# Kernel tuning notes

Hardware: AMD Instinct MI355X
Metric: run time of the kernel (lower is better)

The kernel has to match this reference:

```python
import jax, jax.numpy as jnp
import numpy as np

N_NODES = 100000


def _spmm(edge_src, edge_dst, edge_vals, support):
    # out[i] = sum_{e: dst(e)=i} w_e * support[src(e)]  (sparse adj @ support)
    msgs = support[edge_src] * edge_vals[:, None]  # [E, F]
    return jax.ops.segment_sum(msgs, edge_dst, num_segments=N_NODES)


def setup_inputs() -> dict:
    key = jax.random.key(0)
    ks = jax.random.split(key, 8)
    E = 1600000
    feat_dim, nhid, num_class = 256, 64, 16
    x = jax.random.normal(ks[0], (N_NODES, feat_dim), dtype=jnp.float32)
    edge_src = jax.random.randint(ks[1], (E,), 0, N_NODES, dtype=jnp.int32)
    edge_dst = jax.random.randint(ks[2], (E,), 0, N_NODES, dtype=jnp.int32)
    edge_vals = jax.random.uniform(ks[3], (E,), dtype=jnp.float32)
    # Glorot-style init as in the original GraphConvolution.reset_parameters
    W1 = jax.random.normal(ks[4], (feat_dim, nhid), dtype=jnp.float32) / np.sqrt(feat_dim)
    b1 = jnp.zeros((nhid,), dtype=jnp.float32)
    W2 = jax.random.normal(ks[5], (nhid, num_class), dtype=jnp.float32) / np.sqrt(nhid)
    b2 = jnp.zeros((num_class,), dtype=jnp.float32)
    return {"x": x, "edge_src": edge_src, "edge_dst": edge_dst,
            "edge_vals": edge_vals, "W1": W1, "b1": b1, "W2": W2, "b2": b2}


def reference(x, edge_src, edge_dst, edge_vals, W1, b1, W2, b2):
    # gc1: support = x @ W1 ; out = adj @ support + b1 ; relu
    h = jax.nn.relu(_spmm(edge_src, edge_dst, edge_vals, x @ W1) + b1)
    # dropout is identity in eval mode (training=False)
    # gc2
    logits = _spmm(edge_src, edge_dst, edge_vals, h @ W2) + b2
    return jax.nn.log_softmax(logits, axis=1)
```

## Files before the change

### kernel.cpp

```cpp
#include <hip/hip_runtime.h>
#include <hip/hip_fp16.h>

#define N_NODES 100000
#define E_EDGES 1600000
#define F_IN    256
#define F_HID   64
#define F_OUT   16
#define NBKT    391
#define CAP     4608
#define PA_BLOCKS    391
#define GEMM1_BLOCKS 782

typedef _Float16 half8   __attribute__((ext_vector_type(8)));
typedef float    floatx4 __attribute__((ext_vector_type(4)));

__global__ __launch_bounds__(256) void gemm1_passA_kernel(const float* __restrict__ x,
                                                          const float* __restrict__ W1,
                                                          _Float16* __restrict__ support1,
                                                          const int* __restrict__ esrc,
                                                          const int* __restrict__ edst,
                                                          const float* __restrict__ evals,
                                                          int* __restrict__ bucketCursor,
                                                          int2* __restrict__ tmp) {
    __shared__ __align__(16) char ldsbuf[32768];
    const int t = threadIdx.x;

    if (blockIdx.x >= GEMM1_BLOCKS) {
        int* hist = (int*)ldsbuf;
        int* base = hist + NBKT;
        const int blk = blockIdx.x - GEMM1_BLOCKS;
        for (int i = t; i < NBKT; i += 256) hist[i] = 0;
        __syncthreads();
        const int base_e = blk * 4096;
        int rks[4][4];
#pragma unroll
        for (int ch = 0; ch < 4; ++ch) {
            const int e0 = base_e + ch * 1024 + t * 4;
            if (e0 < E_EDGES) {
                int4 d4 = *(const int4*)&edst[e0];
                rks[ch][0] = atomicAdd(&hist[d4.x >> 8], 1);
                rks[ch][1] = atomicAdd(&hist[d4.y >> 8], 1);
                rks[ch][2] = atomicAdd(&hist[d4.z >> 8], 1);
                rks[ch][3] = atomicAdd(&hist[d4.w >> 8], 1);
            }
        }
        __syncthreads();
        for (int i = t; i < NBKT; i += 256)
            base[i] = atomicAdd(&bucketCursor[i], hist[i]);
        __syncthreads();
#pragma unroll
        for (int ch = 0; ch < 4; ++ch) {
            const int e0 = base_e + ch * 1024 + t * 4;
            if (e0 < E_EDGES) {
                int4 d4 = *(const int4*)&edst[e0];
                int4 s4 = *(const int4*)&esrc[e0];
                float4 v4 = *(const float4*)&evals[e0];
                const int dd[4] = {d4.x, d4.y, d4.z, d4.w};
                const int ss[4] = {s4.x, s4.y, s4.z, s4.w};
                const float vv[4] = {v4.x, v4.y, v4.z, v4.w};
#pragma unroll
                for (int u = 0; u < 4; ++u) {
                    const int bu = dd[u] >> 8;
                    const int bpos = base[bu] + rks[ch][u];
                    if (bpos < CAP)
                        tmp[bu * CAP + bpos] =
                            make_int2(((dd[u] & 255) << 17) | ss[u],
                                      __float_as_int(vv[u]));
                }
            }
        }
        return;
    }

    _Float16* Bs = (_Float16*)ldsbuf;
    for (int i = t; i < 16384; i += 256) {
        const int k = i >> 6, n = i & 63;
        const int kb = k >> 5, quad = (k >> 3) & 3, j = k & 7;
        const int nt = n >> 4, ln = n & 15;
        Bs[((kb * 4 + nt) * 64 + quad * 16 + ln) * 8 + j] = (_Float16)W1[i];
    }
    __syncthreads();

    const int wave = t >> 6;
    const int lane = t & 63;
    const int ln   = lane & 15;
    const int quad = lane >> 4;
    const int row0 = blockIdx.x * 128 + wave * 32;

    const float* xp[2];
#pragma unroll
    for (int mt = 0; mt < 2; ++mt) {
        int r = row0 + mt * 16 + ln;
        if (r > N_NODES - 1) r = N_NODES - 1;
        xp[mt] = x + (size_t)r * F_IN + quad * 8;
    }

    floatx4 acc[2][4] = {};

#pragma unroll 4
    for (int kb = 0; kb < 8; ++kb) {
        half8 a[2];
#pragma unroll
        for (int mt = 0; mt < 2; ++mt) {
            float4 v0 = *(const float4*)(xp[mt] + kb * 32);
            float4 v1 = *(const float4*)(xp[mt] + kb * 32 + 4);
            half8 h;
            h[0] = (_Float16)v0.x; h[1] = (_Float16)v0.y;
            h[2] = (_Float16)v0.z; h[3] = (_Float16)v0.w;
            h[4] = (_Float16)v1.x; h[5] = (_Float16)v1.y;
            h[6] = (_Float16)v1.z; h[7] = (_Float16)v1.w;
            a[mt] = h;
        }
#pragma unroll
        for (int nt = 0; nt < 4; ++nt) {
            half8 b = *(const half8*)&Bs[((size_t)((kb * 4 + nt) * 64 + lane)) * 8];
            acc[0][nt] = __builtin_amdgcn_mfma_f32_16x16x32_f16(a[0], b, acc[0][nt], 0, 0, 0);
            acc[1][nt] = __builtin_amdgcn_mfma_f32_16x16x32_f16(a[1], b, acc[1][nt], 0, 0, 0);
        }
    }

#pragma unroll
    for (int mt = 0; mt < 2; ++mt) {
        const int rbase = row0 + mt * 16 + quad * 4;
#pragma unroll
        for (int r = 0; r < 4; ++r) {
            const int row = rbase + r;
            if (row < N_NODES) {
#pragma unroll
                for (int nt = 0; nt < 4; ++nt)
                    support1[(size_t)row * F_HID + nt * 16 + ln] = (_Float16)acc[mt][nt][r];
            }
        }
    }
}

__global__ __launch_bounds__(256) void passB_kernel(const int2* __restrict__ tmp,
                                                    const int* __restrict__ bucketCursor,
                                                    int2* __restrict__ sorted_edges,
                                                    int* __restrict__ rowstart,
                                                    int* __restrict__ deg) {
    __shared__ int ldeg[256];
    __shared__ int lcur[256];
    __shared__ int s[256];
    const int t = threadIdx.x;
    const int b = blockIdx.x;
    const int beg = b * CAP;
    int cnt = bucketCursor[b];
    if (cnt > CAP) cnt = CAP;

    ldeg[t] = 0;
    __syncthreads();

    for (int p = t; p < cnt; p += 256) {
        int2 r = tmp[beg + p];
        atomicAdd(&ldeg[r.x >> 17], 1);
    }
    __syncthreads();

    const int v = ldeg[t];
    s[t] = v;
    __syncthreads();
#pragma unroll
    for (int off = 1; off < 256; off <<= 1) {
        const int y = (t >= off) ? s[t - off] : 0;
        __syncthreads();
        s[t] += y;
        __syncthreads();
    }
    const int run = s[t] - v;
    lcur[t] = run;
    const int node = b * 256 + t;
    if (node < N_NODES) { rowstart[node] = beg + run; deg[node] = v; }
    __syncthreads();

    for (int p = t; p < cnt; p += 256) {
        int2 r = tmp[beg + p];
        const int pos = beg + atomicAdd(&lcur[r.x >> 17], 1);
        sorted_edges[pos] = make_int2(r.x & 0x1FFFF, r.y);
    }
}

__global__ __launch_bounds__(256) void spmm1_fused_kernel(const int* __restrict__ rowstart,
                                                          const int* __restrict__ deg,
                                                          const int2* __restrict__ sorted_edges,
                                                          const _Float16* __restrict__ support1,
                                                          const float* __restrict__ b1,
                                                          const float* __restrict__ W2,
                                                          _Float16* __restrict__ support2) {
    __shared__ float W2s[64 * 17];
    __shared__ float b1s[64];
    __shared__ __align__(16) float hs[4][64];
    const int t = threadIdx.x;
    for (int i = t; i < 1024; i += 256)
        W2s[(i >> 4) * 17 + (i & 15)] = W2[i];
    if (t < 64) b1s[t] = b1[t];
    __syncthreads();

    const int wave = t >> 6;
    const int lane = t & 63;
    const int node = blockIdx.x * 4 + wave;
    const int c4 = lane & 15;
    const int q  = lane >> 4;

    const int beg = rowstart[node];
    const int cnt = deg[node];

    int   src_l = 0;
    float val_l = 0.f;
    if (lane < cnt) {
        int2 ev = sorted_edges[beg + lane];
        src_l = ev.x;
        val_l = __int_as_float(ev.y);
    }

    float acc0 = 0.f, acc1 = 0.f, acc2 = 0.f, acc3 = 0.f;
    const int kmax  = cnt < 64 ? cnt : 64;
    const int quads = (kmax + 3) >> 2;
    const int qp    = (quads + 3) & ~3;
    for (int k = 0; k < qp; k += 4) {
        float w[4]; uint2 d[4];
#pragma unroll
        for (int u = 0; u < 4; ++u) {
            const int idx = 4 * (k + u) + q;
            const int s2  = __shfl(src_l, idx);
            w[u] = __shfl(val_l, idx);
            d[u] = *(const uint2*)&support1[(size_t)s2 * F_HID + 4 * c4];
        }
#pragma unroll
        for (int u = 0; u < 4; ++u) {
            const _Float16* hp = (const _Float16*)&d[u];
            acc0 = fmaf(w[u], (float)hp[0], acc0);
            acc1 = fmaf(w[u], (float)hp[1], acc1);
            acc2 = fmaf(w[u], (float)hp[2], acc2);
            acc3 = fmaf(w[u], (float)hp[3], acc3);
        }
    }
    for (int k = 64 + q; k < cnt; k += 4) {
        int2 ev = sorted_edges[beg + k];
        const float w = __int_as_float(ev.y);
        const uint2 d = *(const uint2*)&support1[(size_t)ev.x * F_HID + 4 * c4];
        const _Float16* hp = (const _Float16*)&d;
        acc0 = fmaf(w, (float)hp[0], acc0);
        acc1 = fmaf(w, (float)hp[1], acc1);
        acc2 = fmaf(w, (float)hp[2], acc2);
        acc3 = fmaf(w, (float)hp[3], acc3);
    }

    acc0 += __shfl_xor(acc0, 16); acc0 += __shfl_xor(acc0, 32);
    acc1 += __shfl_xor(acc1, 16); acc1 += __shfl_xor(acc1, 32);
    acc2 += __shfl_xor(acc2, 16); acc2 += __shfl_xor(acc2, 32);
    acc3 += __shfl_xor(acc3, 16); acc3 += __shfl_xor(acc3, 32);
    if (q == 0) {
        float4 hv;
        hv.x = fmaxf(acc0 + b1s[4 * c4],     0.f);
        hv.y = fmaxf(acc1 + b1s[4 * c4 + 1], 0.f);
        hv.z = fmaxf(acc2 + b1s[4 * c4 + 2], 0.f);
        hv.w = fmaxf(acc3 + b1s[4 * c4 + 3], 0.f);
        *(float4*)&hs[wave][4 * c4] = hv;
    }
    __syncthreads();

    const int ln   = lane & 15;
    const int quad = lane >> 4;
    float o = 0.f;
#pragma unroll
    for (int kk = 0; kk < 16; ++kk) {
        const int k2 = quad * 16 + kk;
        o = fmaf(hs[wave][k2], W2s[k2 * 17 + ln], o);
    }
    o += __shfl_xor(o, 16);
    o += __shfl_xor(o, 32);
    if (quad == 0)
        support2[(size_t)node * F_OUT + ln] = (_Float16)o;
}

__global__ __launch_bounds__(256) void spmm2_fused_kernel(const int* __restrict__ rowstart,
                                                          const int* __restrict__ deg,
                                                          const int2* __restrict__ sorted_edges,
                                                          const _Float16* __restrict__ support2,
                                                          const float* __restrict__ b2,
                                                          float* __restrict__ out) {
    __shared__ float b2s[16];
    const int t = threadIdx.x;
    if (t < 16) b2s[t] = b2[t];
    __syncthreads();

    const int j    = t & 15;
    const int node = blockIdx.x * 16 + (t >> 4);
    const int c = j & 3;
    const int p = j >> 2;

    const int beg = rowstart[node];
    const int cnt = deg[node];

    int   src_a = 0, src_b = 0;
    float val_a = 0.f, val_b = 0.f;
    if (j < cnt)      { int2 ev = sorted_edges[beg + j];      src_a = ev.x; val_a = __int_as_float(ev.y); }
    if (j + 16 < cnt) { int2 ev = sorted_edges[beg + 16 + j]; src_b = ev.x; val_b = __int_as_float(ev.y); }

    float acc0 = 0.f, acc1 = 0.f, acc2 = 0.f, acc3 = 0.f;
    {
        float w[4]; uint2 d[4];
#pragma unroll
        for (int u = 0; u < 4; ++u) {
            const int idx = 4 * u + p;
            const int s2  = __shfl(src_a, idx, 16);
            w[u] = __shfl(val_a, idx, 16);
            d[u] = *(const uint2*)&support2[(size_t)s2 * F_OUT + 4 * c];
        }
#pragma unroll
        for (int u = 0; u < 4; ++u) {
            const _Float16* hp = (const _Float16*)&d[u];
            acc0 = fmaf(w[u], (float)hp[0], acc0);
            acc1 = fmaf(w[u], (float)hp[1], acc1);
            acc2 = fmaf(w[u], (float)hp[2], acc2);
            acc3 = fmaf(w[u], (float)hp[3], acc3);
        }
    }
    if (cnt > 16) {
        float w[4]; uint2 d[4];
#pragma unroll
        for (int u = 0; u < 4; ++u) {
            const int idx = 4 * u + p;
            const int s2  = __shfl(src_b, idx, 16);
            w[u] = __shfl(val_b, idx, 16);
            d[u] = *(const uint2*)&support2[(size_t)s2 * F_OUT + 4 * c];
        }
#pragma unroll
        for (int u = 0; u < 4; ++u) {
            const _Float16* hp = (const _Float16*)&d[u];
            acc0 = fmaf(w[u], (float)hp[0], acc0);
            acc1 = fmaf(w[u], (float)hp[1], acc1);
            acc2 = fmaf(w[u], (float)hp[2], acc2);
            acc3 = fmaf(w[u], (float)hp[3], acc3);
        }
    }
    for (int k = 32 + p; k < cnt; k += 4) {
        int2 ev = sorted_edges[beg + k];
        const float w = __int_as_float(ev.y);
        const uint2 d = *(const uint2*)&support2[(size_t)ev.x * F_OUT + 4 * c];
        const _Float16* hp = (const _Float16*)&d;
        acc0 = fmaf(w, (float)hp[0], acc0);
        acc1 = fmaf(w, (float)hp[1], acc1);
        acc2 = fmaf(w, (float)hp[2], acc2);
        acc3 = fmaf(w, (float)hp[3], acc3);
    }

    acc0 += __shfl_xor(acc0, 4, 16); acc0 += __shfl_xor(acc0, 8, 16);
    acc1 += __shfl_xor(acc1, 4, 16); acc1 += __shfl_xor(acc1, 8, 16);
    acc2 += __shfl_xor(acc2, 4, 16); acc2 += __shfl_xor(acc2, 8, 16);
    acc3 += __shfl_xor(acc3, 4, 16); acc3 += __shfl_xor(acc3, 8, 16);

    const float v0 = acc0 + b2s[4 * c];
    const float v1 = acc1 + b2s[4 * c + 1];
    const float v2 = acc2 + b2s[4 * c + 2];
    const float v3 = acc3 + b2s[4 * c + 3];
    float m = fmaxf(fmaxf(v0, v1), fmaxf(v2, v3));
    m = fmaxf(m, __shfl_xor(m, 1, 16));
    m = fmaxf(m, __shfl_xor(m, 2, 16));
    float sum = __expf(v0 - m) + __expf(v1 - m) + __expf(v2 - m) + __expf(v3 - m);
    sum += __shfl_xor(sum, 1, 16);
    sum += __shfl_xor(sum, 2, 16);
    if (p == 0) {
        const float lse = m + __logf(sum);
        float4 o = make_float4(v0 - lse, v1 - lse, v2 - lse, v3 - lse);
        *(float4*)&out[(size_t)node * F_OUT + 4 * c] = o;
    }
}

extern "C" void kernel_launch(void* const* d_in, const int* in_sizes, int n_in,
                              void* d_out, int out_size, void* d_ws, size_t ws_size,
                              hipStream_t stream) {
    const float* x     = (const float*)d_in[0];
    const int*   esrc  = (const int*)  d_in[1];
    const int*   edst  = (const int*)  d_in[2];
    const float* evals = (const float*)d_in[3];
    const float* W1    = (const float*)d_in[4];
    const float* b1    = (const float*)d_in[5];
    const float* W2    = (const float*)d_in[6];
    const float* b2    = (const float*)d_in[7];
    float* out = (float*)d_out;

    char* ws = (char*)d_ws;
    _Float16* support1     = (_Float16*)(ws);
    _Float16* support2     = (_Float16*)(ws + 12800000);
    int2*     tmp          = (int2*)    (ws + 16000000);
    int2*     sorted_edges = (int2*)    (ws + 30413824);
    int*      rowstart     = (int*)     (ws + 44827648);
    int*      deg          = (int*)     (ws + 45227648);
    int*      bucketCursor = (int*)     (ws + 45627648);

    hipMemsetAsync(bucketCursor, 0, NBKT * sizeof(int), stream);
    gemm1_passA_kernel<<<GEMM1_BLOCKS + PA_BLOCKS, 256, 0, stream>>>(
        x, W1, support1, esrc, edst, evals, bucketCursor, tmp);
    passB_kernel<<<NBKT, 256, 0, stream>>>(tmp, bucketCursor, sorted_edges, rowstart, deg);
    spmm1_fused_kernel<<<N_NODES / 4, 256, 0, stream>>>(rowstart, deg, sorted_edges,
                                                        support1, b1, W2, support2);
    spmm2_fused_kernel<<<N_NODES / 16, 256, 0, stream>>>(rowstart, deg, sorted_edges,
                                                         support2, b2, out);
}
```

Measured before the change: 294.6 us.

## Replace two-pass bucket sort with global degree count and atomic scatter

The edge sort is restructured. The old version staged edges in a bucketed temporary buffer and then did a second per-bucket local sort. Now per-node degrees are counted with global atomics inside the GEMM1 kernel, a small kernel prefix-sums degrees into row starts within fixed-capacity buckets, and a scatter kernel places each edge directly at its final position with per-node atomic cursors. This removes the temporary buffer write and read and the local histogramming, at the cost of many contended global atomics and an extra kernel launch. Edge order within a row becomes nondeterministic, which can change float summation order.

```diff
diff --git a/kernel.cpp b/kernel.cpp
--- a/kernel.cpp
+++ b/kernel.cpp
@@ -8,68 +8,33 @@
 #define F_OUT   16
 #define NBKT    391
 #define CAP     4608
-#define PA_BLOCKS    391
 #define GEMM1_BLOCKS 782
+#define SC_BLOCKS    1563
 
 typedef _Float16 half8   __attribute__((ext_vector_type(8)));
 typedef float    floatx4 __attribute__((ext_vector_type(4)));
 
-__global__ __launch_bounds__(256) void gemm1_passA_kernel(const float* __restrict__ x,
+__global__ __launch_bounds__(256) void gemm1_count_kernel(const float* __restrict__ x,
                                                           const float* __restrict__ W1,
                                                           _Float16* __restrict__ support1,
-                                                          const int* __restrict__ esrc,
                                                           const int* __restrict__ edst,
-                                                          const float* __restrict__ evals,
-                                                          int* __restrict__ bucketCursor,
-                                                          int2* __restrict__ tmp) {
+                                                          int* __restrict__ deg) {
     __shared__ __align__(16) char ldsbuf[32768];
     const int t = threadIdx.x;
 
-    if (blockIdx.x >= GEMM1_BLOCKS) {
-        int* hist = (int*)ldsbuf;
-        int* base = hist + NBKT;
-        const int blk = blockIdx.x - GEMM1_BLOCKS;
-        for (int i = t; i < NBKT; i += 256) hist[i] = 0;
-        __syncthreads();
-        const int base_e = blk * 4096;
-        int rks[4][4];
-#pragma unroll
-        for (int ch = 0; ch < 4; ++ch) {
+    {
+        const int base_e = blockIdx.x * 2048;
+#pragma unroll
+        for (int ch = 0; ch < 2; ++ch) {
             const int e0 = base_e + ch * 1024 + t * 4;
             if (e0 < E_EDGES) {
                 int4 d4 = *(const int4*)&edst[e0];
-                rks[ch][0] = atomicAdd(&hist[d4.x >> 8], 1);
-                rks[ch][1] = atomicAdd(&hist[d4.y >> 8], 1);
-                rks[ch][2] = atomicAdd(&hist[d4.z >> 8], 1);
-                rks[ch][3] = atomicAdd(&hist[d4.w >> 8], 1);
+                atomicAdd(&deg[d4.x], 1);
+                atomicAdd(&deg[d4.y], 1);
+                atomicAdd(&deg[d4.z], 1);
+                atomicAdd(&deg[d4.w], 1);
             }
         }
-        __syncthreads();
-        for (int i = t; i < NBKT; i += 256)
-            base[i] = atomicAdd(&bucketCursor[i], hist[i]);
-        __syncthreads();
-#pragma unroll
-        for (int ch = 0; ch < 4; ++ch) {
-            const int e0 = base_e + ch * 1024 + t * 4;
-            if (e0 < E_EDGES) {
-                int4 d4 = *(const int4*)&edst[e0];
-                int4 s4 = *(const int4*)&esrc[e0];
-                float4 v4 = *(const float4*)&evals[e0];
-                const int dd[4] = {d4.x, d4.y, d4.z, d4.w};
-                const int ss[4] = {s4.x, s4.y, s4.z, s4.w};
-                const float vv[4] = {v4.x, v4.y, v4.z, v4.w};
-#pragma unroll
-                for (int u = 0; u < 4; ++u) {
-                    const int bu = dd[u] >> 8;
-                    const int bpos = base[bu] + rks[ch][u];
-                    if (bpos < CAP)
-                        tmp[bu * CAP + bpos] =
-                            make_int2(((dd[u] & 255) << 17) | ss[u],
-                                      __float_as_int(vv[u]));
-                }
-            }
-        }
-        return;
     }
 
     _Float16* Bs = (_Float16*)ldsbuf;
@@ -134,30 +99,13 @@
     }
 }
 
-__global__ __launch_bounds__(256) void passB_kernel(const int2* __restrict__ tmp,
-                                                    const int* __restrict__ bucketCursor,
-                                                    int2* __restrict__ sorted_edges,
-                                                    int* __restrict__ rowstart,
-                                                    int* __restrict__ deg) {
-    __shared__ int ldeg[256];
-    __shared__ int lcur[256];
+__global__ __launch_bounds__(256) void rowstart_kernel(int* __restrict__ deg,
+                                                       int* __restrict__ rowstart,
+                                                       int* __restrict__ cur) {
     __shared__ int s[256];
     const int t = threadIdx.x;
-    const int b = blockIdx.x;
-    const int beg = b * CAP;
-    int cnt = bucketCursor[b];
-    if (cnt > CAP) cnt = CAP;
-
-    ldeg[t] = 0;
-    __syncthreads();
-
-    for (int p = t; p < cnt; p += 256) {
-        int2 r = tmp[beg + p];
-        atomicAdd(&ldeg[r.x >> 17], 1);
-    }
-    __syncthreads();
-
-    const int v = ldeg[t];
+    const int node = blockIdx.x * 256 + t;
+    const int v = (node < N_NODES) ? deg[node] : 0;
     s[t] = v;
     __syncthreads();
 #pragma unroll
@@ -167,16 +115,37 @@
         s[t] += y;
         __syncthreads();
     }
-    const int run = s[t] - v;
-    lcur[t] = run;
-    const int node = b * 256 + t;
-    if (node < N_NODES) { rowstart[node] = beg + run; deg[node] = v; }
-    __syncthreads();
-
-    for (int p = t; p < cnt; p += 256) {
-        int2 r = tmp[beg + p];
-        const int pos = beg + atomicAdd(&lcur[r.x >> 17], 1);
-        sorted_edges[pos] = make_int2(r.x & 0x1FFFF, r.y);
+    int run = s[t] - v;
+    if (node < N_NODES) {
+        int degc = v;
+        if (run + v > CAP) degc = (run < CAP) ? (CAP - run) : 0;
+        if (run > CAP) run = CAP;
+        const int rs = blockIdx.x * CAP + run;
+        rowstart[node] = rs;
+        cur[node] = rs;
+        deg[node] = degc;
+    }
+}
+
+__global__ __launch_bounds__(256) void scatter_kernel(const int* __restrict__ esrc,
+                                                      const int* __restrict__ edst,
+                                                      const float* __restrict__ evals,
+                                                      int* __restrict__ cur,
+                                                      int2* __restrict__ sorted_edges) {
+    const int e0 = (blockIdx.x * 256 + threadIdx.x) * 4;
+    if (e0 >= E_EDGES) return;
+    int4 d4 = *(const int4*)&edst[e0];
+    int4 s4 = *(const int4*)&esrc[e0];
+    float4 v4 = *(const float4*)&evals[e0];
+    const int dd[4] = {d4.x, d4.y, d4.z, d4.w};
+    const int ss[4] = {s4.x, s4.y, s4.z, s4.w};
+    const float vv[4] = {v4.x, v4.y, v4.z, v4.w};
+#pragma unroll
+    for (int u = 0; u < 4; ++u) {
+        const int d = dd[u];
+        const int pos = atomicAdd(&cur[d], 1);
+        if (pos < ((d >> 8) + 1) * CAP)
+            sorted_edges[pos] = make_int2(ss[u], __float_as_int(vv[u]));
     }
 }
 
@@ -384,16 +353,15 @@
     char* ws = (char*)d_ws;
     _Float16* support1     = (_Float16*)(ws);
     _Float16* support2     = (_Float16*)(ws + 12800000);
-    int2*     tmp          = (int2*)    (ws + 16000000);
-    int2*     sorted_edges = (int2*)    (ws + 30413824);
-    int*      rowstart     = (int*)     (ws + 44827648);
-    int*      deg          = (int*)     (ws + 45227648);
-    int*      bucketCursor = (int*)     (ws + 45627648);
-
-    hipMemsetAsync(bucketCursor, 0, NBKT * sizeof(int), stream);
-    gemm1_passA_kernel<<<GEMM1_BLOCKS + PA_BLOCKS, 256, 0, stream>>>(
-        x, W1, support1, esrc, edst, evals, bucketCursor, tmp);
-    passB_kernel<<<NBKT, 256, 0, stream>>>(tmp, bucketCursor, sorted_edges, rowstart, deg);
+    int2*     sorted_edges = (int2*)    (ws + 16000000);
+    int*      rowstart     = (int*)     (ws + 30413824);
+    int*      cur          = (int*)     (ws + 30813824);
+    int*      deg          = (int*)     (ws + 31213824);
+
+    hipMemsetAsync(deg, 0, N_NODES * sizeof(int), stream);
+    gemm1_count_kernel<<<GEMM1_BLOCKS, 256, 0, stream>>>(x, W1, support1, edst, deg);
+    rowstart_kernel<<<NBKT, 256, 0, stream>>>(deg, rowstart, cur);
+    scatter_kernel<<<SC_BLOCKS, 256, 0, stream>>>(esrc, edst, evals, cur, sorted_edges);
     spmm1_fused_kernel<<<N_NODES / 4, 256, 0, stream>>>(rowstart, deg, sorted_edges,
                                                         support1, b1, W2, support2);
     spmm2_fused_kernel<<<N_NODES / 16, 256, 0, stream>>>(rowstart, deg, sorted_edges,
```

After: 462.3 us. +56.9%, slower.
